# Kernel tuning notes

Hardware: AMD Instinct MI355X
Metric: run time of the kernel (lower is better)

## Reference

```python
import jax, jax.numpy as jnp
import numpy as np

B, N = 8, 32
V, W_DIM, H_DIM, EMBED, NSTATE = 10000, 512, 512, 256, 30


def _lstm_dir(seq, Wih, Whh, bih, bhh):
    # seq: [M, T, w] -> [M, T, h]; PyTorch gate order i, f, g, o
    M = seq.shape[0]
    H = Whh.shape[1]
    bias = bih + bhh

    def step(carry, x_t):
        h, c = carry
        gates = x_t @ Wih.T + h @ Whh.T + bias
        i, f, g, o = jnp.split(gates, 4, axis=-1)
        c = jax.nn.sigmoid(f) * c + jax.nn.sigmoid(i) * jnp.tanh(g)
        h = jax.nn.sigmoid(o) * jnp.tanh(c)
        return (h, c), h

    init = (jnp.zeros((M, H), seq.dtype), jnp.zeros((M, H), seq.dtype))
    _, hs = jax.lax.scan(step, init, jnp.swapaxes(seq, 0, 1))
    return jnp.swapaxes(hs, 0, 1)


def setup_inputs() -> dict:
    key = jax.random.key(0)
    ks = jax.random.split(key, 8)
    sc = 1.0 / np.sqrt(H_DIM)
    nrm = lambda k, shape, s: jax.random.normal(k, shape, dtype=jnp.float32) * s
    return {
        "x": jax.random.randint(ks[0], (B, N), 0, V, dtype=jnp.int32),
        "lengths": jnp.full((B,), N, dtype=jnp.int32),
        "emb": nrm(ks[1], (V, W_DIM), 0.02),
        "Wih_f": nrm(ks[2], (4 * H_DIM, W_DIM), sc),
        "Whh_f": nrm(ks[3], (4 * H_DIM, H_DIM), sc),
        "bih_f": jnp.zeros((4 * H_DIM,), jnp.float32),
        "bhh_f": jnp.zeros((4 * H_DIM,), jnp.float32),
        "Wih_b": nrm(ks[4], (4 * H_DIM, W_DIM), sc),
        "Whh_b": nrm(ks[5], (4 * H_DIM, H_DIM), sc),
        "bih_b": jnp.zeros((4 * H_DIM,), jnp.float32),
        "bhh_b": jnp.zeros((4 * H_DIM,), jnp.float32),
        "Wout": nrm(ks[6], (NSTATE * EMBED, 2 * H_DIM), 1.0 / np.sqrt(2 * H_DIM)),
        "bout": jnp.zeros((NSTATE * EMBED,), jnp.float32),
    }


def reference(x, lengths, emb, Wih_f, Whh_f, bih_f, bhh_f,
              Wih_b, Whh_b, bih_b, bhh_b, Wout, bout):
    word_emb = emb[x]  # [B, N, w]
    chunks = []
    for k in range(1, N):  # loop over span lengths, as in the original
        # windows of length k+1 starting at each position: [N-k, k+1]
        idx = jnp.arange(k + 1)[None, :] + jnp.arange(N - k)[:, None]
        span = word_emb[:, idx].reshape(B * (N - k), k + 1, W_DIM)
        fwd = _lstm_dir(span, Wih_f, Whh_f, bih_f, bhh_f)
        bwd = _lstm_dir(span[:, ::-1], Wih_b, Whh_b, bih_b, bhh_b)[:, ::-1]
        h = jnp.concatenate([fwd, bwd], axis=-1)  # [M, k+1, 2h]
        out = h @ Wout.T + bout                   # [M, k+1, NSTATE*EMBED]
        out = out.reshape(B, N - k, k + 1, NSTATE, EMBED).mean(axis=2)
        chunks.append(out)
    # spans laid out by increasing length: [B, N(N-1)/2, NSTATE, EMBED]
    return jnp.concatenate(chunks, axis=1)
```

## Files before the change

kernel.cpp:

```cpp
#include <hip/hip_runtime.h>
#include <hip/hip_bf16.h>


#define BT __hip_bfloat16

typedef short bf16x8 __attribute__((ext_vector_type(8)));
typedef float f32x4 __attribute__((ext_vector_type(4)));

__device__ __forceinline__ bf16x8 ld_frag(const BT* p) {
    return *reinterpret_cast<const bf16x8*>(p);
}
__device__ __forceinline__ f32x4 mfma16(bf16x8 a, bf16x8 b, f32x4 c) {
    return __builtin_amdgcn_mfma_f32_16x16x32_bf16(a, b, c, 0, 0, 0);
}
__device__ __forceinline__ float sigm(float x) { return 1.0f / (1.0f + __expf(-x)); }
__device__ __forceinline__ float tanhfast(float x) {
    float e = __expf(-2.0f * fabsf(x));
    float r = (1.0f - e) / (1.0f + e);
    return copysignf(r, x);
}

__device__ __forceinline__ bf16x8 ld_sys16(const BT* p) {
    bf16x8 r;
    asm volatile("global_load_dwordx4 %0, %1, off sc0 sc1"
                 : "=v"(r) : "v"(p) : "memory");
    return r;
}
__device__ __forceinline__ void st_sys_short(BT* p, BT v) {
    union { BT b; unsigned short u; } t; t.b = v;
    unsigned int d = t.u;
    asm volatile("global_store_short %0, %1, off sc0 sc1"
                 :: "v"(p), "v"(d) : "memory");
}
__device__ __forceinline__ void st_sys_u32(unsigned int* p, unsigned int v) {
    asm volatile("global_store_dword %0, %1, off sc0 sc1"
                 :: "v"(p), "v"(v) : "memory");
}
__device__ __forceinline__ unsigned int ld_sys_u32(const unsigned int* p) {
    unsigned int r;
    asm volatile("global_load_dword %0, %1, off sc0 sc1\n\t"
                 "s_waitcnt vmcnt(0)"
                 : "=v"(r) : "v"(p) : "memory");
    return r;
}

__device__ __forceinline__ void async16(const BT* g, BT* l) {
    __builtin_amdgcn_global_load_lds(
        (const __attribute__((address_space(1))) unsigned int*)g,
        (__attribute__((address_space(3))) unsigned int*)l,
        16, 0, 0);
}

union B4 { BT b[4]; unsigned long long u; };

__global__ __launch_bounds__(256) void conv_kernel(
    const float* __restrict__ s0, const float* __restrict__ s1,
    const float* __restrict__ s2, const float* __restrict__ s3,
    const float* __restrict__ s4, BT* __restrict__ dbase)
{
    const int z = blockIdx.z;
    const float* src = (z == 0) ? s0 : (z == 1) ? s1 : (z == 2) ? s2 : (z == 3) ? s3 : s4;
    const int nel = (z == 4) ? 7864320 : 1048576;
    BT* dst = dbase + (long)z * 1048576;
    const int n4 = nel >> 2;
    for (int i = blockIdx.x * 256 + threadIdx.x; i < n4; i += gridDim.x * 256) {
        float4 v = reinterpret_cast<const float4*>(src)[i];
        B4 t;
        t.b[0] = __float2bfloat16(v.x); t.b[1] = __float2bfloat16(v.y);
        t.b[2] = __float2bfloat16(v.z); t.b[3] = __float2bfloat16(v.w);
        reinterpret_cast<unsigned long long*>(dst)[i] = t.u;
    }
}

__global__ __launch_bounds__(256) void gather_kernel(
    const int* __restrict__ x, const float* __restrict__ emb, BT* __restrict__ Xemb)
{
    const int i = blockIdx.x * 256 + threadIdx.x;
    const int r = i >> 7;
    const int cq = i & 127;
    const long row = x[r];
    float4 v = reinterpret_cast<const float4*>(emb + row * 512)[cq];
    B4 t;
    t.b[0] = __float2bfloat16(v.x); t.b[1] = __float2bfloat16(v.y);
    t.b[2] = __float2bfloat16(v.z); t.b[3] = __float2bfloat16(v.w);
    reinterpret_cast<unsigned long long*>(Xemb + (long)r * 512)[cq] = t.u;
}

__global__ __launch_bounds__(256) void gx_kernel(
    const BT* __restrict__ Xemb,
    const BT* __restrict__ WihF, const BT* __restrict__ WihB,
    const float* __restrict__ bih_f, const float* __restrict__ bhh_f,
    const float* __restrict__ bih_b, const float* __restrict__ bhh_b,
    float* __restrict__ Gx, unsigned int* __restrict__ flags)
{
    const int dir = blockIdx.z;
    const BT* Wih = dir ? WihB : WihF;
    const float* bih = dir ? bih_b : bih_f;
    const float* bhh = dir ? bhh_b : bhh_f;
    float* G = Gx + (long)dir * 256 * 2048;

    const int tid = threadIdx.x;
    const int w = tid >> 6, lane = tid & 63;
    const int m = lane & 15, q = lane >> 4;
    const int r0 = blockIdx.x * 32;
    const int c0 = blockIdx.y * 128 + w * 32;

    if (tid == 0)
        st_sys_u32(&flags[(blockIdx.z * 8 + blockIdx.x) * 16 + blockIdx.y], 0u);

    const BT* a0p = Xemb + (long)(r0 + m) * 512 + q * 8;
    const BT* a1p = Xemb + (long)(r0 + 16 + m) * 512 + q * 8;
    const BT* b0p = Wih + (long)(c0 + m) * 512 + q * 8;
    const BT* b1p = Wih + (long)(c0 + 16 + m) * 512 + q * 8;

    f32x4 acc[2][2] = {};
    for (int k0 = 0; k0 < 512; k0 += 32) {
        bf16x8 a0 = ld_frag(a0p + k0);
        bf16x8 a1 = ld_frag(a1p + k0);
        bf16x8 b0 = ld_frag(b0p + k0);
        bf16x8 b1 = ld_frag(b1p + k0);
        acc[0][0] = mfma16(a0, b0, acc[0][0]);
        acc[0][1] = mfma16(a0, b1, acc[0][1]);
        acc[1][0] = mfma16(a1, b0, acc[1][0]);
        acc[1][1] = mfma16(a1, b1, acc[1][1]);
    }
    #pragma unroll
    for (int rt = 0; rt < 2; ++rt)
        #pragma unroll
        for (int ct = 0; ct < 2; ++ct)
            #pragma unroll
            for (int reg = 0; reg < 4; ++reg) {
                int r = r0 + rt * 16 + q * 4 + reg;
                int c = c0 + ct * 16 + m;
                G[(long)r * 2048 + c] = acc[rt][ct][reg] + bih[c] + bhh[c];
            }
}

__global__ __launch_bounds__(256, 1) void rec_kernel(
    const BT* __restrict__ WhhF, const BT* __restrict__ WhhB,
    const float* __restrict__ Gx,
    BT* __restrict__ H0, BT* __restrict__ H1,
    float* __restrict__ C, float* __restrict__ S,
    BT* __restrict__ Apack, unsigned int* __restrict__ flags)
{
    const int dir = blockIdx.z;
    const int tid = threadIdx.x;
    const int w = tid >> 6, lane = tid & 63;
    const int m = lane & 15, q = lane >> 4;

    const BT* W = dir ? WhhB : WhhF;
    const float* G = Gx + (long)dir * 256 * 2048;
    BT* Ha = H0 + (long)dir * 256 * 512;
    BT* Hb = H1 + (long)dir * 256 * 512;
    float* Cd = C + (long)dir * 256 * 512;
    float* Sd = S + (long)dir * 256 * 512;

    const int r0 = blockIdx.x * 32;
    const int u0 = blockIdx.y * 32;
    unsigned int* flg = flags + (dir * 8 + blockIdx.x) * 16;
    const int myy = blockIdx.y;

    const BT* b0p = W + (long)(w * 512 + u0 + m) * 512 + q * 8;
    const BT* b1p = W + (long)(w * 512 + u0 + 16 + m) * 512 + q * 8;
    bf16x8 wb0[16], wb1[16];
    #pragma unroll
    for (int kk = 0; kk < 16; ++kk) {
        wb0[kk] = ld_frag(b0p + kk * 32);
        wb1[kk] = ld_frag(b1p + kk * 32);
    }

    __shared__ float gbuf[4][32][33];
    __shared__ BT hbuf[32 * 512];

    const int srow = tid >> 3;
    const int sch0 = tid & 7;
    const int xr = m & 7;

    for (int s = 0; s < 32; ++s) {
        const BT* Hi = (s & 1) ? Hb : Ha;
        BT* Ho = (s & 1) ? Ha : Hb;
        const bool active = (r0 < 8 * (s + 1));
        const int pos = dir ? (31 - s) : s;
        float hreg[4];

        if (active) {
            const BT* hsrc = Hi + (long)(r0 + srow) * 512;
            bf16x8 hv[8];
            #pragma unroll
            for (int rr = 0; rr < 8; ++rr)
                hv[rr] = ld_sys16(hsrc + (sch0 + rr * 8) * 8);
            asm volatile("s_waitcnt vmcnt(0)" ::: "memory");
            __builtin_amdgcn_sched_barrier(0);
            #pragma unroll
            for (int rr = 0; rr < 8; ++rr) {
                const int ch = sch0 + rr * 8;
                *reinterpret_cast<bf16x8*>(
                    hbuf + srow * 512 + (ch ^ (srow & 7)) * 8) = hv[rr];
            }
            __syncthreads();

            f32x4 acc[2][2] = {};
            #pragma unroll
            for (int kk = 0; kk < 16; ++kk) {
                const int sl = (((kk << 2) | q) ^ xr) * 8;
                bf16x8 a0 = *reinterpret_cast<const bf16x8*>(hbuf + m * 512 + sl);
                bf16x8 a1 = *reinterpret_cast<const bf16x8*>(hbuf + (16 + m) * 512 + sl);
                acc[0][0] = mfma16(a0, wb0[kk], acc[0][0]);
                acc[0][1] = mfma16(a0, wb1[kk], acc[0][1]);
                acc[1][0] = mfma16(a1, wb0[kk], acc[1][0]);
                acc[1][1] = mfma16(a1, wb1[kk], acc[1][1]);
            }
            #pragma unroll
            for (int rt = 0; rt < 2; ++rt)
                #pragma unroll
                for (int ct = 0; ct < 2; ++ct)
                    #pragma unroll
                    for (int reg = 0; reg < 4; ++reg)
                        gbuf[w][rt * 16 + q * 4 + reg][ct * 16 + m] = acc[rt][ct][reg];
            __syncthreads();

            #pragma unroll
            for (int j = 0; j < 4; ++j) {
                const int idx = tid + j * 256;
                const int r = idx >> 5, ul = idx & 31;
                const int chain = r0 + r;
                const int d = chain >> 3;
                const int b = chain & 7;
                if (d > s) continue;
                const int u = u0 + ul;
                const float* gx = G + (long)(b * 32 + pos) * 2048 + u;
                const float gi = gbuf[0][r][ul] + gx[0];
                const float gf = gbuf[1][r][ul] + gx[512];
                const float gg = gbuf[2][r][ul] + gx[1024];
                const float go = gbuf[3][r][ul] + gx[1536];
                const long o = (long)chain * 512 + u;
                const float c_new = sigm(gf) * Cd[o] + sigm(gi) * tanhfast(gg);
                const float h = sigm(go) * tanhfast(c_new);
                Cd[o] = c_new;
                st_sys_short(Ho + o, __float2bfloat16(h));
                hreg[j] = h;
            }
        }

        if (s < 31) {
            asm volatile("s_waitcnt vmcnt(0)" ::: "memory");
            __syncthreads();
            if (tid == 0)
                st_sys_u32(&flg[myy], (unsigned)(s + 1));
        }

        if (active) {
            #pragma unroll
            for (int j = 0; j < 4; ++j) {
                const int idx = tid + j * 256;
                const int r = idx >> 5, ul = idx & 31;
                const int chain = r0 + r;
                const int d = chain >> 3;
                const int b = chain & 7;
                if (d > s) continue;
                const int u = u0 + ul;
                const long o = (long)chain * 512 + u;
                const float s_new = Sd[o] + hreg[j];
                Sd[o] = s_new;
                const int k = s - d;
                if (k >= 1) {
                    const int p_span = dir ? pos : d;
                    const int off = (k - 1) * 32 - ((k - 1) * k) / 2;
                    Apack[(long)(b * 496 + off + p_span) * 1024 + dir * 512 + u] =
                        __float2bfloat16(s_new * __builtin_amdgcn_rcpf((float)(k + 1)));
                }
            }
        }

        if (s < 31) {
            if (tid < 16) {
                const unsigned int tgt = (unsigned)(s + 1);
                while (ld_sys_u32(&flg[tid]) < tgt)
                    __builtin_amdgcn_s_sleep(1);
            }
            __syncthreads();
            asm volatile("" ::: "memory");
        }
    }
}

__global__ __launch_bounds__(256) void proj_kernel(
    const BT* __restrict__ Apack, const BT* __restrict__ Woutbf,
    const float* __restrict__ bout, float* __restrict__ out)
{
    __shared__ BT As[128 * 64];
    __shared__ BT Bs[128 * 64];

    const int tid = threadIdx.x;
    const int lane = tid & 63;
    const int wu = __builtin_amdgcn_readfirstlane(tid >> 6);
    const int m = lane & 15, q = lane >> 4;
    const int wr = wu >> 1, wc = wu & 1;
    const int r0 = blockIdx.x * 128;
    const int c0 = blockIdx.y * 128;

    const int srow = lane >> 3;
    const int schunk = (lane & 7) ^ srow;

    f32x4 acc[4][4] = {};

    for (int kc = 0; kc < 16; ++kc) {
        const int k0 = kc * 64;
        #pragma unroll
        for (int j = 0; j < 4; ++j) {
            const int L = wu * 4 + j;
            const int row = L * 8 + srow;
            async16(Apack + (long)(r0 + row) * 1024 + k0 + schunk * 8,
                    As + L * 512);
            async16(Woutbf + (long)(c0 + row) * 1024 + k0 + schunk * 8,
                    Bs + L * 512);
        }
        __syncthreads();
        #pragma unroll
        for (int ks = 0; ks < 2; ++ks) {
            const int slot = ((ks << 2) | q) ^ (m & 7);
            bf16x8 af[4], bf[4];
            #pragma unroll
            for (int t = 0; t < 4; ++t) {
                af[t] = ld_frag(As + (wr * 64 + t * 16 + m) * 64 + slot * 8);
                bf[t] = ld_frag(Bs + (wc * 64 + t * 16 + m) * 64 + slot * 8);
            }
            #pragma unroll
            for (int mt = 0; mt < 4; ++mt)
                #pragma unroll
                for (int nt = 0; nt < 4; ++nt)
                    acc[mt][nt] = mfma16(af[mt], bf[nt], acc[mt][nt]);
        }
        __syncthreads();
    }

    #pragma unroll
    for (int mt = 0; mt < 4; ++mt)
        #pragma unroll
        for (int nt = 0; nt < 4; ++nt)
            #pragma unroll
            for (int reg = 0; reg < 4; ++reg) {
                const int r = r0 + wr * 64 + mt * 16 + q * 4 + reg;
                const int c = c0 + wc * 64 + nt * 16 + m;
                out[(long)r * 7680 + c] = acc[mt][nt][reg] + bout[c];
            }
}

extern "C" void kernel_launch(void* const* d_in, const int* in_sizes, int n_in,
                              void* d_out, int out_size, void* d_ws, size_t ws_size,
                              hipStream_t stream) {
    const int*   x     = (const int*)d_in[0];
    const float* emb   = (const float*)d_in[2];
    const float* Wih_f = (const float*)d_in[3];
    const float* Whh_f = (const float*)d_in[4];
    const float* bih_f = (const float*)d_in[5];
    const float* bhh_f = (const float*)d_in[6];
    const float* Wih_b = (const float*)d_in[7];
    const float* Whh_b = (const float*)d_in[8];
    const float* bih_b = (const float*)d_in[9];
    const float* bhh_b = (const float*)d_in[10];
    const float* Wout  = (const float*)d_in[11];
    const float* bout  = (const float*)d_in[12];
    float* out = (float*)d_out;

    char* ws = (char*)d_ws;
    const long MB = 1 << 20;
    float* Gx    = (float*)(ws + 0);
    BT*    H0    = (BT*)(ws + 4 * MB);
    BT*    H1    = (BT*)(ws + 4 * MB + 512 * 1024);
    float* C     = (float*)(ws + 5 * MB);
    float* S     = (float*)(ws + 6 * MB);
    BT*    Apack = (BT*)(ws + 7 * MB);
    BT*    Xemb  = (BT*)(ws + 7 * MB + 7936 * 1024);
    BT*    Wbf   = (BT*)(ws + 15 * MB);
    BT*    WihF  = Wbf;
    BT*    WihB  = Wbf + 1048576;
    BT*    WhhF  = Wbf + 2 * 1048576;
    BT*    WhhB  = Wbf + 3 * 1048576;
    BT*    Woutb = Wbf + 4 * 1048576;
    unsigned int* flags = (unsigned int*)(ws + 38 * MB);

    hipMemsetAsync(ws + 4 * MB, 0, 3 * MB, stream);

    conv_kernel<<<dim3(512, 1, 5), 256, 0, stream>>>(
        Wih_f, Wih_b, Whh_f, Whh_b, Wout, Wbf);
    gather_kernel<<<128, 256, 0, stream>>>(x, emb, Xemb);

    gx_kernel<<<dim3(8, 16, 2), 256, 0, stream>>>(
        Xemb, WihF, WihB, bih_f, bhh_f, bih_b, bhh_b, Gx, flags);

    rec_kernel<<<dim3(8, 16, 2), 256, 0, stream>>>(
        WhhF, WhhB, Gx, H0, H1, C, S, Apack, flags);

    proj_kernel<<<dim3(31, 60), 256, 0, stream>>>(Apack, Woutb, bout, out);
}
```

Before: 456.1 us.

## Keep LSTM cell/sum state in registers, vectorize epilogue, fuse prep kernels, remap proj blocks

The recurrent kernel now holds the cell state and running h-sum in registers per thread. It processes 4 contiguous units with float4 loads and 64-bit stores, which removes global C/S arrays and their per-step read/write traffic, and the memset shrinks to match. The embedding gather is folded into the weight-conversion kernel to save a launch. The projection GEMM remaps block IDs so that consecutive tiles land on the same XCD, aiming for better L2 reuse. The gbuf padding changes to 36 to allow aligned float4 LDS reads, which may add bank conflicts.

```diff
diff --git a/kernel.cpp b/kernel.cpp
--- a/kernel.cpp
+++ b/kernel.cpp
@@ -26,11 +26,9 @@
                  : "=v"(r) : "v"(p) : "memory");
     return r;
 }
-__device__ __forceinline__ void st_sys_short(BT* p, BT v) {
-    union { BT b; unsigned short u; } t; t.b = v;
-    unsigned int d = t.u;
-    asm volatile("global_store_short %0, %1, off sc0 sc1"
-                 :: "v"(p), "v"(d) : "memory");
+__device__ __forceinline__ void st_sys_u64(void* p, unsigned long long v) {
+    asm volatile("global_store_dwordx2 %0, %1, off sc0 sc1"
+                 :: "v"(p), "v"(v) : "memory");
 }
 __device__ __forceinline__ void st_sys_u32(unsigned int* p, unsigned int v) {
     asm volatile("global_store_dword %0, %1, off sc0 sc1"
@@ -52,13 +50,30 @@
 }
 
 union B4 { BT b[4]; unsigned long long u; };
-
-__global__ __launch_bounds__(256) void conv_kernel(
+union F4 { float4 v; float f[4]; };
+
+__global__ __launch_bounds__(256) void prep_kernel(
     const float* __restrict__ s0, const float* __restrict__ s1,
     const float* __restrict__ s2, const float* __restrict__ s3,
-    const float* __restrict__ s4, BT* __restrict__ dbase)
+    const float* __restrict__ s4, BT* __restrict__ dbase,
+    const int* __restrict__ x, const float* __restrict__ emb,
+    BT* __restrict__ Xemb)
 {
     const int z = blockIdx.z;
+    if (z == 5) {
+        const int i = blockIdx.x * 256 + threadIdx.x;
+        if (i < 32768) {
+            const int r = i >> 7;
+            const int cq = i & 127;
+            const long row = x[r];
+            float4 v = reinterpret_cast<const float4*>(emb + row * 512)[cq];
+            B4 t;
+            t.b[0] = __float2bfloat16(v.x); t.b[1] = __float2bfloat16(v.y);
+            t.b[2] = __float2bfloat16(v.z); t.b[3] = __float2bfloat16(v.w);
+            reinterpret_cast<unsigned long long*>(Xemb + (long)r * 512)[cq] = t.u;
+        }
+        return;
+    }
     const float* src = (z == 0) ? s0 : (z == 1) ? s1 : (z == 2) ? s2 : (z == 3) ? s3 : s4;
     const int nel = (z == 4) ? 7864320 : 1048576;
     BT* dst = dbase + (long)z * 1048576;
@@ -70,20 +85,6 @@
         t.b[2] = __float2bfloat16(v.z); t.b[3] = __float2bfloat16(v.w);
         reinterpret_cast<unsigned long long*>(dst)[i] = t.u;
     }
-}
-
-__global__ __launch_bounds__(256) void gather_kernel(
-    const int* __restrict__ x, const float* __restrict__ emb, BT* __restrict__ Xemb)
-{
-    const int i = blockIdx.x * 256 + threadIdx.x;
-    const int r = i >> 7;
-    const int cq = i & 127;
-    const long row = x[r];
-    float4 v = reinterpret_cast<const float4*>(emb + row * 512)[cq];
-    B4 t;
-    t.b[0] = __float2bfloat16(v.x); t.b[1] = __float2bfloat16(v.y);
-    t.b[2] = __float2bfloat16(v.z); t.b[3] = __float2bfloat16(v.w);
-    reinterpret_cast<unsigned long long*>(Xemb + (long)r * 512)[cq] = t.u;
 }
 
 __global__ __launch_bounds__(256) void gx_kernel(
@@ -140,7 +141,6 @@
     const BT* __restrict__ WhhF, const BT* __restrict__ WhhB,
     const float* __restrict__ Gx,
     BT* __restrict__ H0, BT* __restrict__ H1,
-    float* __restrict__ C, float* __restrict__ S,
     BT* __restrict__ Apack, unsigned int* __restrict__ flags)
 {
     const int dir = blockIdx.z;
@@ -152,8 +152,6 @@
     const float* G = Gx + (long)dir * 256 * 2048;
     BT* Ha = H0 + (long)dir * 256 * 512;
     BT* Hb = H1 + (long)dir * 256 * 512;
-    float* Cd = C + (long)dir * 256 * 512;
-    float* Sd = S + (long)dir * 256 * 512;
 
     const int r0 = blockIdx.x * 32;
     const int u0 = blockIdx.y * 32;
@@ -169,19 +167,26 @@
         wb1[kk] = ld_frag(b1p + kk * 32);
     }
 
-    __shared__ float gbuf[4][32][33];
+    __shared__ float gbuf[4][32][36];
     __shared__ BT hbuf[32 * 512];
 
     const int srow = tid >> 3;
     const int sch0 = tid & 7;
     const int xr = m & 7;
+
+    const int er = tid >> 3;
+    const int eu4 = (tid & 7) * 4;
+    const int echain = r0 + er;
+    const int ed = echain >> 3, eb = echain & 7;
+    const int eu = u0 + eu4;
+    float creg[4] = {}, sreg[4] = {};
 
     for (int s = 0; s < 32; ++s) {
         const BT* Hi = (s & 1) ? Hb : Ha;
         BT* Ho = (s & 1) ? Ha : Hb;
         const bool active = (r0 < 8 * (s + 1));
+        const bool ework = active && (ed <= s);
         const int pos = dir ? (31 - s) : s;
-        float hreg[4];
 
         if (active) {
             const BT* hsrc = Hi + (long)(r0 + srow) * 512;
@@ -219,26 +224,31 @@
                         gbuf[w][rt * 16 + q * 4 + reg][ct * 16 + m] = acc[rt][ct][reg];
             __syncthreads();
 
-            #pragma unroll
-            for (int j = 0; j < 4; ++j) {
-                const int idx = tid + j * 256;
-                const int r = idx >> 5, ul = idx & 31;
-                const int chain = r0 + r;
-                const int d = chain >> 3;
-                const int b = chain & 7;
-                if (d > s) continue;
-                const int u = u0 + ul;
-                const float* gx = G + (long)(b * 32 + pos) * 2048 + u;
-                const float gi = gbuf[0][r][ul] + gx[0];
-                const float gf = gbuf[1][r][ul] + gx[512];
-                const float gg = gbuf[2][r][ul] + gx[1024];
-                const float go = gbuf[3][r][ul] + gx[1536];
-                const long o = (long)chain * 512 + u;
-                const float c_new = sigm(gf) * Cd[o] + sigm(gi) * tanhfast(gg);
-                const float h = sigm(go) * tanhfast(c_new);
-                Cd[o] = c_new;
-                st_sys_short(Ho + o, __float2bfloat16(h));
-                hreg[j] = h;
+            if (ework) {
+                const float* gxp = G + (long)(eb * 32 + pos) * 2048 + eu;
+                F4 xi, xf, xg, xo, hi4, hf4, hg4, ho4;
+                xi.v = *(const float4*)(gxp);
+                xf.v = *(const float4*)(gxp + 512);
+                xg.v = *(const float4*)(gxp + 1024);
+                xo.v = *(const float4*)(gxp + 1536);
+                hi4.v = *(const float4*)&gbuf[0][er][eu4];
+                hf4.v = *(const float4*)&gbuf[1][er][eu4];
+                hg4.v = *(const float4*)&gbuf[2][er][eu4];
+                ho4.v = *(const float4*)&gbuf[3][er][eu4];
+                B4 hp;
+                #pragma unroll
+                for (int jj = 0; jj < 4; ++jj) {
+                    const float gi = hi4.f[jj] + xi.f[jj];
+                    const float gf = hf4.f[jj] + xf.f[jj];
+                    const float gg = hg4.f[jj] + xg.f[jj];
+                    const float go = ho4.f[jj] + xo.f[jj];
+                    const float c_new = sigm(gf) * creg[jj] + sigm(gi) * tanhfast(gg);
+                    const float h = sigm(go) * tanhfast(c_new);
+                    creg[jj] = c_new;
+                    sreg[jj] += h;
+                    hp.b[jj] = __float2bfloat16(h);
+                }
+                st_sys_u64(Ho + (long)echain * 512 + eu, hp.u);
             }
         }
 
@@ -249,26 +259,18 @@
                 st_sys_u32(&flg[myy], (unsigned)(s + 1));
         }
 
-        if (active) {
-            #pragma unroll
-            for (int j = 0; j < 4; ++j) {
-                const int idx = tid + j * 256;
-                const int r = idx >> 5, ul = idx & 31;
-                const int chain = r0 + r;
-                const int d = chain >> 3;
-                const int b = chain & 7;
-                if (d > s) continue;
-                const int u = u0 + ul;
-                const long o = (long)chain * 512 + u;
-                const float s_new = Sd[o] + hreg[j];
-                Sd[o] = s_new;
-                const int k = s - d;
-                if (k >= 1) {
-                    const int p_span = dir ? pos : d;
-                    const int off = (k - 1) * 32 - ((k - 1) * k) / 2;
-                    Apack[(long)(b * 496 + off + p_span) * 1024 + dir * 512 + u] =
-                        __float2bfloat16(s_new * __builtin_amdgcn_rcpf((float)(k + 1)));
-                }
+        if (ework) {
+            const int k = s - ed;
+            if (k >= 1) {
+                const float inv = __builtin_amdgcn_rcpf((float)(k + 1));
+                B4 ap;
+                #pragma unroll
+                for (int jj = 0; jj < 4; ++jj)
+                    ap.b[jj] = __float2bfloat16(sreg[jj] * inv);
+                const int p_span = dir ? pos : ed;
+                const int off = (k - 1) * 32 - ((k - 1) * k) / 2;
+                *reinterpret_cast<unsigned long long*>(
+                    Apack + (long)(eb * 496 + off + p_span) * 1024 + dir * 512 + eu) = ap.u;
             }
         }
 
@@ -296,8 +298,14 @@
     const int wu = __builtin_amdgcn_readfirstlane(tid >> 6);
     const int m = lane & 15, q = lane >> 4;
     const int wr = wu >> 1, wc = wu & 1;
-    const int r0 = blockIdx.x * 128;
-    const int c0 = blockIdx.y * 128;
+
+    int id = blockIdx.x + 31 * blockIdx.y;
+    const int qq = 232, rr = 4;
+    const int xcd = id & 7, rank = id >> 3;
+    id = (xcd < rr) ? (xcd * (qq + 1) + rank)
+                    : (rr * (qq + 1) + (xcd - rr) * qq + rank);
+    const int r0 = (id % 31) * 128;
+    const int c0 = (id / 31) * 128;
 
     const int srow = lane >> 3;
     const int schunk = (lane & 7) ^ srow;
@@ -368,8 +376,6 @@
     float* Gx    = (float*)(ws + 0);
     BT*    H0    = (BT*)(ws + 4 * MB);
     BT*    H1    = (BT*)(ws + 4 * MB + 512 * 1024);
-    float* C     = (float*)(ws + 5 * MB);
-    float* S     = (float*)(ws + 6 * MB);
     BT*    Apack = (BT*)(ws + 7 * MB);
     BT*    Xemb  = (BT*)(ws + 7 * MB + 7936 * 1024);
     BT*    Wbf   = (BT*)(ws + 15 * MB);
@@ -380,17 +386,16 @@
     BT*    Woutb = Wbf + 4 * 1048576;
     unsigned int* flags = (unsigned int*)(ws + 38 * MB);
 
-    hipMemsetAsync(ws + 4 * MB, 0, 3 * MB, stream);
-
-    conv_kernel<<<dim3(512, 1, 5), 256, 0, stream>>>(
-        Wih_f, Wih_b, Whh_f, Whh_b, Wout, Wbf);
-    gather_kernel<<<128, 256, 0, stream>>>(x, emb, Xemb);
+    hipMemsetAsync(ws + 4 * MB, 0, 1 * MB, stream);
+
+    prep_kernel<<<dim3(512, 1, 6), 256, 0, stream>>>(
+        Wih_f, Wih_b, Whh_f, Whh_b, Wout, Wbf, x, emb, Xemb);
 
     gx_kernel<<<dim3(8, 16, 2), 256, 0, stream>>>(
         Xemb, WihF, WihB, bih_f, bhh_f, bih_b, bhh_b, Gx, flags);
 
     rec_kernel<<<dim3(8, 16, 2), 256, 0, stream>>>(
-        WhhF, WhhB, Gx, H0, H1, C, S, Apack, flags);
+        WhhF, WhhB, Gx, H0, H1, Apack, flags);
 
     proj_kernel<<<dim3(31, 60), 256, 0, stream>>>(Apack, Woutb, bout, out);
 }
```

New measurement: 411.5 us. -9.8%, faster.
